# Kernel tuning notes

Measured on AMD Instinct MI355X. Metric: run time of the kernel, lower is better.

Reference implementation:

```python
import jax, jax.numpy as jnp
import numpy as np

LOCAL_K = 3
TOKEN_T, TOKEN_H, TOKEN_W = 8, 32, 32  # N = T*H*W = 8192
HIDDEN, N_HEADS = 256, 8


def _gather_neighbors(kv):
    # kv: [B, N, D2] -> [B, N, 27, D2] of 3x3x3 neighborhood (zero padded)
    B, N, D2 = kv.shape
    pad = LOCAL_K // 2
    x3d = kv.reshape(B, TOKEN_T, TOKEN_H, TOKEN_W, D2)
    x3d = jnp.pad(x3d, ((0, 0), (pad, pad), (pad, pad), (pad, pad), (0, 0)))
    slices = [
        x3d[:, dt:dt + TOKEN_T, dh:dh + TOKEN_H, dw:dw + TOKEN_W, :]
        for dt in range(LOCAL_K)
        for dh in range(LOCAL_K)
        for dw in range(LOCAL_K)
    ]
    nb = jnp.stack(slices, axis=4)  # [B, T, H, W, 27, D2]
    return nb.reshape(B, N, LOCAL_K ** 3, D2)


def setup_inputs() -> dict:
    key = jax.random.key(0)
    k1, k2, k3 = jax.random.split(key, 3)
    B, N, D = 2, TOKEN_T * TOKEN_H * TOKEN_W, HIDDEN
    x = jax.random.normal(k1, (B, N, D), dtype=jnp.float32)
    w_qkv = jax.random.normal(k2, (3 * D, D), dtype=jnp.float32) * (D ** -0.5)
    w_out = jax.random.normal(k3, (D, D), dtype=jnp.float32) * (D ** -0.5)
    return {"x": x, "w_qkv": w_qkv, "w_out": w_out}


def reference(x, w_qkv, w_out):
    B, N, D = x.shape
    H, d = N_HEADS, D // N_HEADS
    qkv = x @ w_qkv.T                       # [B, N, 3D]
    q, k, v = jnp.split(qkv, 3, axis=-1)
    kv_nb = _gather_neighbors(jnp.concatenate([k, v], axis=-1))  # [B,N,27,2D]
    k_nb, v_nb = jnp.split(kv_nb, 2, axis=-1)
    q = q.reshape(B, N, H, d)
    k_nb = k_nb.reshape(B, N, 27, H, d)
    v_nb = v_nb.reshape(B, N, 27, H, d)
    scale = 1.0 / jnp.sqrt(jnp.asarray(d, dtype=q.dtype))
    scores = jnp.einsum('bnhd,bnkhd->bnhk', q, k_nb) * scale  # [B,N,H,27]
    attn = jax.nn.softmax(scores, axis=-1)
    out = jnp.einsum('bnhk,bnkhd->bnhd', attn, v_nb)           # [B,N,H,d]
    return out.reshape(B, N, D) @ w_out.T
```

## Files before the change

kernel.cpp:

```cpp
#include <hip/hip_runtime.h>
#include <hip/hip_bf16.h>

#define TOK_T 8
#define TOK_H 32
#define TOK_W 32
#define NTOK 8192
#define BATCH 2
#define DMODEL 256
#define D3 768
#define NHEADS 8
#define DHEAD 32

using short8  = __attribute__((ext_vector_type(8))) short;
using ushort8 = __attribute__((ext_vector_type(8))) unsigned short;
using f32x4   = __attribute__((ext_vector_type(4))) float;

__device__ __forceinline__ ushort f2bf(float f) {
  union { float f; unsigned u; } v; v.f = f;
  unsigned u = v.u;
  unsigned r = (u + 0x7FFFu + ((u >> 16) & 1u)) >> 16;
  return (ushort)r;
}
__device__ __forceinline__ float bf2f(ushort u) {
  union { unsigned u; float f; } v; v.u = ((unsigned)u) << 16;
  return v.f;
}

#define NX4  (BATCH * NTOK * DMODEL / 4)
#define NW14 (D3 * DMODEL / 4)
#define NW24 (DMODEL * DMODEL / 4)

__global__ __launch_bounds__(256) void convert_all(const float* __restrict__ x,
                                                   const float* __restrict__ wq,
                                                   const float* __restrict__ wo,
                                                   ushort* __restrict__ xb,
                                                   ushort* __restrict__ wqb,
                                                   ushort* __restrict__ wob) {
  int i = blockIdx.x * 256 + threadIdx.x;
  const float* src; ushort* dst; int j;
  if (i < NX4)              { src = x;  dst = xb;  j = i; }
  else if (i < NX4 + NW14)  { src = wq; dst = wqb; j = i - NX4; }
  else if (i < NX4 + NW14 + NW24) { src = wo; dst = wob; j = i - NX4 - NW14; }
  else return;
  float4 v = ((const float4*)src)[j];
  ushort4 o;
  o.x = f2bf(v.x); o.y = f2bf(v.y); o.z = f2bf(v.z); o.w = f2bf(v.w);
  ((ushort4*)dst)[j] = o;
}

#define BM 128
#define BN 128
#define BKK 32

template<bool OUT_BF16>
__global__ __launch_bounds__(256) void gemm_bt(const ushort* __restrict__ A,
                                               const ushort* __restrict__ B,
                                               void* __restrict__ Cv,
                                               int M, int N, int K) {
  __shared__ __align__(16) ushort sA[2][BM * BKK];
  __shared__ __align__(16) ushort sB[2][BN * BKK];
  const int tid  = threadIdx.x;
  const int lane = tid & 63;
  const int wid  = tid >> 6;
  const int wr   = wid >> 1;
  const int wc   = wid & 1;
  const int bm   = blockIdx.x * BM;
  const int bn   = blockIdx.y * BN;
  const int fr   = lane & 15;
  const int kb   = lane >> 4;

  f32x4 acc[4][4] = {};

  auto stage = [&](int buf, int kt) {
#pragma unroll
    for (int j = 0; j < 2; ++j) {
      int c  = wid * 128 + j * 64 + lane;
      int r  = c >> 2;
      int sl = c & 3;
      int ss = sl ^ ((r >> 1) & 3);
      const ushort* srcA = A + (size_t)(bm + r) * K + kt + ss * 8;
      const ushort* srcB = B + (size_t)(bn + r) * K + kt + ss * 8;
      ushort* dstA = &sA[buf][(wid * 128 + j * 64) * 8];
      ushort* dstB = &sB[buf][(wid * 128 + j * 64) * 8];
      __builtin_amdgcn_global_load_lds((const __attribute__((address_space(1))) void*)srcA,
                                       (__attribute__((address_space(3))) void*)dstA, 16, 0, 0);
      __builtin_amdgcn_global_load_lds((const __attribute__((address_space(1))) void*)srcB,
                                       (__attribute__((address_space(3))) void*)dstB, 16, 0, 0);
    }
  };

  const int nit = K >> 5;
  stage(0, 0);
  __syncthreads();

  for (int it = 0; it < nit; ++it) {
    const int cur = it & 1;
    if (it + 1 < nit) stage(cur ^ 1, (it + 1) << 5);

    short8 af[4], bfr[4];
#pragma unroll
    for (int m = 0; m < 4; ++m) {
      int r  = wr * 64 + m * 16 + fr;
      int ck = r * 4 + (kb ^ ((r >> 1) & 3));
      af[m] = *(const short8*)&sA[cur][ck * 8];
    }
#pragma unroll
    for (int n = 0; n < 4; ++n) {
      int r  = wc * 64 + n * 16 + fr;
      int ck = r * 4 + (kb ^ ((r >> 1) & 3));
      bfr[n] = *(const short8*)&sB[cur][ck * 8];
    }
#pragma unroll
    for (int m = 0; m < 4; ++m)
#pragma unroll
      for (int n = 0; n < 4; ++n)
        acc[m][n] = __builtin_amdgcn_mfma_f32_16x16x32_bf16(af[m], bfr[n], acc[m][n], 0, 0, 0);
    __syncthreads();
  }

  if constexpr (OUT_BF16) {
    ushort* C = (ushort*)Cv;
#pragma unroll
    for (int m = 0; m < 4; ++m)
#pragma unroll
      for (int n = 0; n < 4; ++n)
#pragma unroll
        for (int j = 0; j < 4; ++j) {
          int row = bm + wr * 64 + m * 16 + kb * 4 + j;
          int col = bn + wc * 64 + n * 16 + fr;
          C[(size_t)row * N + col] = f2bf(acc[m][n][j]);
        }
  } else {
    float* C = (float*)Cv;
#pragma unroll
    for (int m = 0; m < 4; ++m)
#pragma unroll
      for (int n = 0; n < 4; ++n)
#pragma unroll
        for (int j = 0; j < 4; ++j) {
          int row = bm + wr * 64 + m * 16 + kb * 4 + j;
          int col = bn + wc * 64 + n * 16 + fr;
          C[(size_t)row * N + col] = acc[m][n][j];
        }
  }
}

#define TT 2
#define TLH 8
#define TLW 8
#define NHALO 400
#define KP 40

__global__ __launch_bounds__(128) void local_attn(const ushort* __restrict__ qkv,
                                                  ushort* __restrict__ aob) {
  __shared__ __align__(16) ushort sh[NHALO * KP];
  const int tile = blockIdx.x;
  const int head = blockIdx.y;
  const int b    = blockIdx.z;
  const int tz = tile >> 4;
  const int ty = (tile >> 2) & 3;
  const int tx = tile & 3;
  const int t0 = tz * TT, h0 = ty * TLH, w0 = tx * TLW;
  const int tid = threadIdx.x;

  auto stage = [&](int ofs) {
    for (int idx = tid; idx < NHALO; idx += 128) {
      int ht  = idx / 100;
      int rem = idx - ht * 100;
      int hh  = rem / 10;
      int hw  = rem - hh * 10;
      int gt = t0 - 1 + ht, gh = h0 - 1 + hh, gw = w0 - 1 + hw;
      ushort8* dst = (ushort8*)&sh[idx * KP];
      if (gt >= 0 && gt < TOK_T && gh >= 0 && gh < TOK_H && gw >= 0 && gw < TOK_W) {
        size_t base = ((size_t)b * NTOK + (size_t)gt * 1024 + gh * 32 + gw) * D3;
        const ushort8* s = (const ushort8*)(qkv + base + ofs + head * DHEAD);
#pragma unroll
        for (int p = 0; p < 4; ++p) dst[p] = s[p];
      } else {
        ushort8 z = (ushort8)0;
#pragma unroll
        for (int p = 0; p < 4; ++p) dst[p] = z;
      }
    }
  };

  stage(DMODEL);

  const int tt = tid >> 6;
  const int th = (tid >> 3) & 7;
  const int tw = tid & 7;
  const int n  = (t0 + tt) * 1024 + (h0 + th) * 32 + (w0 + tw);

  const ushort* qp = qkv + ((size_t)b * NTOK + n) * D3 + head * DHEAD;
  float q[DHEAD];
  {
    const ushort8* qs = (const ushort8*)qp;
#pragma unroll
    for (int p = 0; p < 4; ++p) {
      ushort8 v = qs[p];
#pragma unroll
      for (int e = 0; e < 8; ++e) q[p * 8 + e] = bf2f(v[e]);
    }
  }
  __syncthreads();

  const float scale = 0.1767766952966369f;
  float s[27];
#pragma unroll
  for (int nb = 0; nb < 27; ++nb) {
    int dt = nb / 9, dh = (nb / 3) % 3, dw = nb % 3;
    int hidx = (tt + dt) * 100 + (th + dh) * 10 + (tw + dw);
    const ushort8* kp = (const ushort8*)&sh[hidx * KP];
    float a = 0.f;
#pragma unroll
    for (int p = 0; p < 4; ++p) {
      ushort8 kk = kp[p];
#pragma unroll
      for (int e = 0; e < 8; ++e) a += q[p * 8 + e] * bf2f(kk[e]);
    }
    s[nb] = a * scale;
  }
  __syncthreads();

  stage(2 * DMODEL);

  float mx = s[0];
#pragma unroll
  for (int nb = 1; nb < 27; ++nb) mx = fmaxf(mx, s[nb]);
  __syncthreads();

  float o[DHEAD] = {};
  float sum = 0.f;
#pragma unroll
  for (int nb = 0; nb < 27; ++nb) {
    int dt = nb / 9, dh = (nb / 3) % 3, dw = nb % 3;
    int hidx = (tt + dt) * 100 + (th + dh) * 10 + (tw + dw);
    const ushort8* vp = (const ushort8*)&sh[hidx * KP];
    float p = __expf(s[nb] - mx);
    sum += p;
#pragma unroll
    for (int c = 0; c < 4; ++c) {
      ushort8 vv = vp[c];
#pragma unroll
      for (int e = 0; e < 8; ++e) o[c * 8 + e] += p * bf2f(vv[e]);
    }
  }

  float inv = 1.f / sum;
  ushort8 os[4];
#pragma unroll
  for (int c = 0; c < 4; ++c)
#pragma unroll
    for (int e = 0; e < 8; ++e) os[c][e] = f2bf(o[c * 8 + e] * inv);
  ushort8* op = (ushort8*)(aob + ((size_t)b * NTOK + n) * DMODEL + head * DHEAD);
#pragma unroll
  for (int c = 0; c < 4; ++c) op[c] = os[c];
}

extern "C" void kernel_launch(void* const* d_in, const int* in_sizes, int n_in,
                              void* d_out, int out_size, void* d_ws, size_t ws_size,
                              hipStream_t stream) {
  const float* x     = (const float*)d_in[0];
  const float* w_qkv = (const float*)d_in[1];
  const float* w_out = (const float*)d_in[2];
  float* out = (float*)d_out;

  char* ws = (char*)d_ws;
  size_t off = 0;
  ushort* xb    = (ushort*)(ws + off); off += (size_t)BATCH * NTOK * DMODEL * 2;
  ushort* wqkvb = (ushort*)(ws + off); off += (size_t)D3 * DMODEL * 2;
  ushort* woutb = (ushort*)(ws + off); off += (size_t)DMODEL * DMODEL * 2;
  ushort* qkvb  = (ushort*)(ws + off); off += (size_t)BATCH * NTOK * D3 * 2;
  ushort* aob   = (ushort*)(ws + off); off += (size_t)BATCH * NTOK * DMODEL * 2;

  int ntot = NX4 + NW14 + NW24;
  convert_all<<<(ntot + 255) / 256, 256, 0, stream>>>(x, w_qkv, w_out, xb, wqkvb, woutb);

  dim3 g1(BATCH * NTOK / BM, D3 / BN);
  gemm_bt<true><<<g1, 256, 0, stream>>>(xb, wqkvb, (void*)qkvb, BATCH * NTOK, D3, DMODEL);

  dim3 ga(64, NHEADS, BATCH);
  local_attn<<<ga, 128, 0, stream>>>(qkvb, aob);

  dim3 g2(BATCH * NTOK / BM, DMODEL / BN);
  gemm_bt<false><<<g2, 256, 0, stream>>>(aob, woutb, (void*)out, BATCH * NTOK, DMODEL, DMODEL);
}
```

Baseline: 67.39 us.

## Fuse conversion, QKV GEMM, local attention and output GEMM into one cooperative kernel

Replaces four kernel launches with one persistent cooperative kernel of 256 blocks that uses grid-wide syncs between the QKV projection, neighbourhood attention and output projection phases. The fp32-to-bf16 conversion of x and the weights now happens inline as GEMM tiles are loaded into shared memory, removing the separate conversion pass and its bf16 copies in memory. GEMM tiles are reshaped to 128x128 computed by 512 threads, and the attention tiles grow to 4x8x8 tokens with a 600-token halo. This removes launch gaps and intermediate traffic, at the cost of only one 512-thread block per CU, grid-sync overhead, and register-staged loads instead of direct global-to-LDS loads.

```diff
diff --git a/kernel.cpp b/kernel.cpp
--- a/kernel.cpp
+++ b/kernel.cpp
@@ -1,5 +1,8 @@
 #include <hip/hip_runtime.h>
 #include <hip/hip_bf16.h>
+#include <hip/hip_cooperative_groups.h>
+
+namespace cg = cooperative_groups;
 
 #define TOK_T 8
 #define TOK_H 32
@@ -26,149 +29,138 @@
   return v.f;
 }
 
-#define NX4  (BATCH * NTOK * DMODEL / 4)
-#define NW14 (D3 * DMODEL / 4)
-#define NW24 (DMODEL * DMODEL / 4)
-
-__global__ __launch_bounds__(256) void convert_all(const float* __restrict__ x,
-                                                   const float* __restrict__ wq,
-                                                   const float* __restrict__ wo,
-                                                   ushort* __restrict__ xb,
-                                                   ushort* __restrict__ wqb,
-                                                   ushort* __restrict__ wob) {
-  int i = blockIdx.x * 256 + threadIdx.x;
-  const float* src; ushort* dst; int j;
-  if (i < NX4)              { src = x;  dst = xb;  j = i; }
-  else if (i < NX4 + NW14)  { src = wq; dst = wqb; j = i - NX4; }
-  else if (i < NX4 + NW14 + NW24) { src = wo; dst = wob; j = i - NX4 - NW14; }
-  else return;
-  float4 v = ((const float4*)src)[j];
-  ushort4 o;
-  o.x = f2bf(v.x); o.y = f2bf(v.y); o.z = f2bf(v.z); o.w = f2bf(v.w);
-  ((ushort4*)dst)[j] = o;
-}
-
-#define BM 128
-#define BN 128
-#define BKK 32
-
-template<bool OUT_BF16>
-__global__ __launch_bounds__(256) void gemm_bt(const ushort* __restrict__ A,
-                                               const ushort* __restrict__ B,
-                                               void* __restrict__ Cv,
-                                               int M, int N, int K) {
-  __shared__ __align__(16) ushort sA[2][BM * BKK];
-  __shared__ __align__(16) ushort sB[2][BN * BKK];
+template<bool AF32, bool BF32, bool OUTBF16>
+__device__ __forceinline__ void gemm128(const void* __restrict__ Av,
+                                        const void* __restrict__ Bv,
+                                        void* __restrict__ Cv,
+                                        int bm, int bn, int ldc,
+                                        ushort* __restrict__ sm) {
   const int tid  = threadIdx.x;
   const int lane = tid & 63;
   const int wid  = tid >> 6;
   const int wr   = wid >> 1;
   const int wc   = wid & 1;
-  const int bm   = blockIdx.x * BM;
-  const int bn   = blockIdx.y * BN;
   const int fr   = lane & 15;
   const int kb   = lane >> 4;
-
-  f32x4 acc[4][4] = {};
-
-  auto stage = [&](int buf, int kt) {
-#pragma unroll
-    for (int j = 0; j < 2; ++j) {
-      int c  = wid * 128 + j * 64 + lane;
-      int r  = c >> 2;
-      int sl = c & 3;
-      int ss = sl ^ ((r >> 1) & 3);
-      const ushort* srcA = A + (size_t)(bm + r) * K + kt + ss * 8;
-      const ushort* srcB = B + (size_t)(bn + r) * K + kt + ss * 8;
-      ushort* dstA = &sA[buf][(wid * 128 + j * 64) * 8];
-      ushort* dstB = &sB[buf][(wid * 128 + j * 64) * 8];
-      __builtin_amdgcn_global_load_lds((const __attribute__((address_space(1))) void*)srcA,
-                                       (__attribute__((address_space(3))) void*)dstA, 16, 0, 0);
-      __builtin_amdgcn_global_load_lds((const __attribute__((address_space(1))) void*)srcB,
-                                       (__attribute__((address_space(3))) void*)dstB, 16, 0, 0);
+  const int sr   = tid >> 2;
+  const int sk   = tid & 3;
+  const int sck  = sr * 4 + (sk ^ ((sr >> 1) & 3));
+
+  f32x4 acc[2][4] = {};
+
+  float4 a0, a1, b0, b1;
+  ushort8 a16, b16;
+
+  auto load = [&](int kt) {
+    if constexpr (AF32) {
+      const float* Ap = (const float*)Av + (size_t)(bm + sr) * 256 + kt + sk * 8;
+      a0 = *(const float4*)Ap;
+      a1 = *(const float4*)(Ap + 4);
+    } else {
+      a16 = *(const ushort8*)((const ushort*)Av + (size_t)(bm + sr) * 256 + kt + sk * 8);
+    }
+    if constexpr (BF32) {
+      const float* Bp = (const float*)Bv + (size_t)(bn + sr) * 256 + kt + sk * 8;
+      b0 = *(const float4*)Bp;
+      b1 = *(const float4*)(Bp + 4);
+    } else {
+      b16 = *(const ushort8*)((const ushort*)Bv + (size_t)(bn + sr) * 256 + kt + sk * 8);
     }
   };
-
-  const int nit = K >> 5;
-  stage(0, 0);
-  __syncthreads();
-
-  for (int it = 0; it < nit; ++it) {
+  auto stow = [&](int buf) {
+    ushort8 av, bv;
+    if constexpr (AF32) {
+      av[0] = f2bf(a0.x); av[1] = f2bf(a0.y); av[2] = f2bf(a0.z); av[3] = f2bf(a0.w);
+      av[4] = f2bf(a1.x); av[5] = f2bf(a1.y); av[6] = f2bf(a1.z); av[7] = f2bf(a1.w);
+    } else av = a16;
+    if constexpr (BF32) {
+      bv[0] = f2bf(b0.x); bv[1] = f2bf(b0.y); bv[2] = f2bf(b0.z); bv[3] = f2bf(b0.w);
+      bv[4] = f2bf(b1.x); bv[5] = f2bf(b1.y); bv[6] = f2bf(b1.z); bv[7] = f2bf(b1.w);
+    } else bv = b16;
+    *(ushort8*)&sm[buf * 8192 + sck * 8] = av;
+    *(ushort8*)&sm[buf * 8192 + 4096 + sck * 8] = bv;
+  };
+
+  load(0);
+  stow(0);
+  __syncthreads();
+
+  for (int it = 0; it < 8; ++it) {
     const int cur = it & 1;
-    if (it + 1 < nit) stage(cur ^ 1, (it + 1) << 5);
-
-    short8 af[4], bfr[4];
-#pragma unroll
-    for (int m = 0; m < 4; ++m) {
-      int r  = wr * 64 + m * 16 + fr;
+    if (it < 7) load((it + 1) * 32);
+
+    short8 af[2], bf8[4];
+#pragma unroll
+    for (int m = 0; m < 2; ++m) {
+      int r  = wr * 32 + m * 16 + fr;
       int ck = r * 4 + (kb ^ ((r >> 1) & 3));
-      af[m] = *(const short8*)&sA[cur][ck * 8];
+      af[m] = *(const short8*)&sm[cur * 8192 + ck * 8];
     }
 #pragma unroll
     for (int n = 0; n < 4; ++n) {
       int r  = wc * 64 + n * 16 + fr;
       int ck = r * 4 + (kb ^ ((r >> 1) & 3));
-      bfr[n] = *(const short8*)&sB[cur][ck * 8];
-    }
-#pragma unroll
-    for (int m = 0; m < 4; ++m)
+      bf8[n] = *(const short8*)&sm[cur * 8192 + 4096 + ck * 8];
+    }
+#pragma unroll
+    for (int m = 0; m < 2; ++m)
 #pragma unroll
       for (int n = 0; n < 4; ++n)
-        acc[m][n] = __builtin_amdgcn_mfma_f32_16x16x32_bf16(af[m], bfr[n], acc[m][n], 0, 0, 0);
+        acc[m][n] = __builtin_amdgcn_mfma_f32_16x16x32_bf16(af[m], bf8[n], acc[m][n], 0, 0, 0);
+
+    if (it < 7) stow(cur ^ 1);
     __syncthreads();
   }
 
-  if constexpr (OUT_BF16) {
+  if constexpr (OUTBF16) {
     ushort* C = (ushort*)Cv;
 #pragma unroll
-    for (int m = 0; m < 4; ++m)
+    for (int m = 0; m < 2; ++m)
 #pragma unroll
       for (int n = 0; n < 4; ++n)
 #pragma unroll
         for (int j = 0; j < 4; ++j) {
-          int row = bm + wr * 64 + m * 16 + kb * 4 + j;
+          int row = bm + wr * 32 + m * 16 + kb * 4 + j;
           int col = bn + wc * 64 + n * 16 + fr;
-          C[(size_t)row * N + col] = f2bf(acc[m][n][j]);
+          C[(size_t)row * ldc + col] = f2bf(acc[m][n][j]);
         }
   } else {
     float* C = (float*)Cv;
 #pragma unroll
-    for (int m = 0; m < 4; ++m)
+    for (int m = 0; m < 2; ++m)
 #pragma unroll
       for (int n = 0; n < 4; ++n)
 #pragma unroll
         for (int j = 0; j < 4; ++j) {
-          int row = bm + wr * 64 + m * 16 + kb * 4 + j;
+          int row = bm + wr * 32 + m * 16 + kb * 4 + j;
           int col = bn + wc * 64 + n * 16 + fr;
-          C[(size_t)row * N + col] = acc[m][n][j];
+          C[(size_t)row * ldc + col] = acc[m][n][j];
         }
   }
 }
 
-#define TT 2
-#define TLH 8
-#define TLW 8
-#define NHALO 400
+#define NHALO 600
 #define KP 40
 
-__global__ __launch_bounds__(128) void local_attn(const ushort* __restrict__ qkv,
-                                                  ushort* __restrict__ aob) {
-  __shared__ __align__(16) ushort sh[NHALO * KP];
-  const int tile = blockIdx.x;
-  const int head = blockIdx.y;
-  const int b    = blockIdx.z;
+__device__ __forceinline__ void attn_unit(const ushort* __restrict__ qkv,
+                                          ushort* __restrict__ aob,
+                                          int unit, int stid,
+                                          ushort* __restrict__ sh) {
+  const int b    = unit >> 8;
+  const int rem  = unit & 255;
+  const int head = rem >> 5;
+  const int tile = rem & 31;
   const int tz = tile >> 4;
   const int ty = (tile >> 2) & 3;
   const int tx = tile & 3;
-  const int t0 = tz * TT, h0 = ty * TLH, w0 = tx * TLW;
-  const int tid = threadIdx.x;
+  const int t0 = tz * 4, h0 = ty * 8, w0 = tx * 8;
 
   auto stage = [&](int ofs) {
-    for (int idx = tid; idx < NHALO; idx += 128) {
+    for (int idx = stid; idx < NHALO; idx += 256) {
       int ht  = idx / 100;
-      int rem = idx - ht * 100;
-      int hh  = rem / 10;
-      int hw  = rem - hh * 10;
+      int rem2 = idx - ht * 100;
+      int hh  = rem2 / 10;
+      int hw  = rem2 - hh * 10;
       int gt = t0 - 1 + ht, gh = h0 - 1 + hh, gw = w0 - 1 + hw;
       ushort8* dst = (ushort8*)&sh[idx * KP];
       if (gt >= 0 && gt < TOK_T && gh >= 0 && gh < TOK_H && gw >= 0 && gw < TOK_W) {
@@ -186,9 +178,9 @@
 
   stage(DMODEL);
 
-  const int tt = tid >> 6;
-  const int th = (tid >> 3) & 7;
-  const int tw = tid & 7;
+  const int tt = stid >> 6;
+  const int th = (stid >> 3) & 7;
+  const int tw = stid & 7;
   const int n  = (t0 + tt) * 1024 + (h0 + th) * 32 + (w0 + tw);
 
   const ushort* qp = qkv + ((size_t)b * NTOK + n) * D3 + head * DHEAD;
@@ -255,6 +247,30 @@
   ushort8* op = (ushort8*)(aob + ((size_t)b * NTOK + n) * DMODEL + head * DHEAD);
 #pragma unroll
   for (int c = 0; c < 4; ++c) op[c] = os[c];
+}
+
+__global__ __launch_bounds__(512, 1) void mega(const float* __restrict__ x,
+                                               const float* __restrict__ wq,
+                                               const float* __restrict__ wo,
+                                               ushort* __restrict__ qkv,
+                                               ushort* __restrict__ aob,
+                                               float* __restrict__ out) {
+  __shared__ __align__(16) ushort sm[48000];
+  const int blk = blockIdx.x;
+  cg::grid_group grid = cg::this_grid();
+
+#pragma unroll 1
+  for (int r = 0; r < 3; ++r) {
+    int u = blk * 3 + r;
+    gemm128<true, true, true>(x, wq, qkv, (u / 6) * 128, (u % 6) * 128, D3, sm);
+  }
+  grid.sync();
+
+  attn_unit(qkv, aob, blk * 2 + (threadIdx.x >> 8), threadIdx.x & 255,
+            sm + (threadIdx.x >> 8) * (NHALO * KP));
+  grid.sync();
+
+  gemm128<false, true, false>(aob, wo, out, (blk >> 1) * 128, (blk & 1) * 128, DMODEL, sm);
 }
 
 extern "C" void kernel_launch(void* const* d_in, const int* in_sizes, int n_in,
@@ -266,22 +282,10 @@
   float* out = (float*)d_out;
 
   char* ws = (char*)d_ws;
-  size_t off = 0;
-  ushort* xb    = (ushort*)(ws + off); off += (size_t)BATCH * NTOK * DMODEL * 2;
-  ushort* wqkvb = (ushort*)(ws + off); off += (size_t)D3 * DMODEL * 2;
-  ushort* woutb = (ushort*)(ws + off); off += (size_t)DMODEL * DMODEL * 2;
-  ushort* qkvb  = (ushort*)(ws + off); off += (size_t)BATCH * NTOK * D3 * 2;
-  ushort* aob   = (ushort*)(ws + off); off += (size_t)BATCH * NTOK * DMODEL * 2;
-
-  int ntot = NX4 + NW14 + NW24;
-  convert_all<<<(ntot + 255) / 256, 256, 0, stream>>>(x, w_qkv, w_out, xb, wqkvb, woutb);
-
-  dim3 g1(BATCH * NTOK / BM, D3 / BN);
-  gemm_bt<true><<<g1, 256, 0, stream>>>(xb, wqkvb, (void*)qkvb, BATCH * NTOK, D3, DMODEL);
-
-  dim3 ga(64, NHEADS, BATCH);
-  local_attn<<<ga, 128, 0, stream>>>(qkvb, aob);
-
-  dim3 g2(BATCH * NTOK / BM, DMODEL / BN);
-  gemm_bt<false><<<g2, 256, 0, stream>>>(aob, woutb, (void*)out, BATCH * NTOK, DMODEL, DMODEL);
-}
+  ushort* qkvb = (ushort*)ws;
+  ushort* aob  = (ushort*)(ws + (size_t)BATCH * NTOK * D3 * 2);
+
+  void* args[6] = {(void*)&x, (void*)&w_qkv, (void*)&w_out,
+                   (void*)&qkvb, (void*)&aob, (void*)&out};
+  hipLaunchCooperativeKernel((const void*)mega, dim3(256), dim3(512), args, 0u, stream);
+}
```

After: 194.7 us. 189% more time.
